# Kernel optimization log

Hardware: AMD Instinct MI355X
Metric: run time of the kernel (lower is better)

## Reference

```python
import jax, jax.numpy as jnp
import numpy as np

N_UNITS = 2048
N_INPUTS = 16
BATCH = 64
T = 512
PROP_EXC = 0.8
TAU = 5.0
GLOBAL_NOISE_LEVEL = 0.01
NOISE_CONST = float(np.sqrt(2.0 * GLOBAL_NOISE_LEVEL / TAU))


def setup_inputs() -> dict:
    key = jax.random.key(0)
    ks = jax.random.split(key, 7)
    inputs = jax.random.normal(ks[0], (BATCH, N_INPUTS, T), dtype=jnp.float32)
    noise = NOISE_CONST * jax.random.normal(ks[1], (T, BATCH, N_UNITS), dtype=jnp.float32)
    # parameters (match torch.rand-based init distributions)
    inp = jax.random.uniform(ks[2], (N_INPUTS, N_UNITS), dtype=jnp.float32)
    Wrecnon = (jax.random.uniform(ks[3], (N_UNITS, N_UNITS), dtype=jnp.float32) - 1.0) / N_UNITS
    Wrecdale = jax.random.uniform(ks[4], (N_UNITS, N_UNITS), dtype=jnp.float32) / N_UNITS
    out_w = jax.random.uniform(ks[5], (N_UNITS, 1), dtype=jnp.float32)
    alpha = jnp.array([0.5], dtype=jnp.float32)
    n_exc = int(PROP_EXC * N_UNITS)
    sdale = jnp.where(jnp.arange(N_UNITS) < n_exc, 1.0, -1.0).astype(jnp.float32)  # diag of Sdale
    return {"inputs": inputs, "noise": noise, "inp": inp, "Wrecnon": Wrecnon,
            "Wrecdale": Wrecdale, "out_w": out_w, "alpha": alpha, "sdale": sdale}


def reference(inputs, noise, inp, Wrecnon, Wrecdale, out_w, alpha, sdale):
    prop_old = 1.0 - 1.0 / TAU
    prop_new = 1.0 / TAU
    use_alpha = jnp.clip(alpha, 0.0, 1.0)  # Hardtanh(0, 1)
    # Wsum = a * |Wrecdale| @ diag(sdale) + (1 - a) * Wrecnon
    Wsum = use_alpha * (jnp.abs(Wrecdale) * sdale[None, :]) + (1.0 - use_alpha) * Wrecnon
    inp_abs = jnp.abs(inp)  # [n_inputs, n_units]
    x_seq = jnp.transpose(inputs, (2, 0, 1))  # [T, B, n_inputs]

    def step(activity, xs):
        x_t, n_t = xs
        # matmul(Wsum, relu(act)[..., None]).squeeze() == relu(act) @ Wsum.T
        drive = jnp.maximum(activity, 0.0) @ Wsum.T + x_t @ inp_abs
        activity = prop_old * activity + prop_new * drive + n_t
        return activity, None

    activity0 = jnp.zeros((inputs.shape[0], Wsum.shape[0]), dtype=inputs.dtype)
    activity, _ = jax.lax.scan(step, activity0, (x_seq, noise))
    output = (activity @ out_w)[:, 0]  # [B]
    return output, activity
```

## Files before the change

kernel.cpp:

```cpp
#include <hip/hip_runtime.h>

#define N_UNITS 2048
#define N_IN 16
#define BATCH 64
#define T_STEPS 512

typedef __attribute__((ext_vector_type(8))) short bf16x8;
typedef __attribute__((ext_vector_type(4))) float f32x4;
typedef __attribute__((ext_vector_type(4))) unsigned short u16x4;

#define AP_OFF   0
#define BX_OFF   17039360
#define BR0_OFF  21233664
#define BR1_OFF  21757952
#define ACT_OFF  22282240

__device__ __forceinline__ unsigned short f2bf(float f) {
  unsigned int u = __float_as_uint(f);
  u += 0x7FFFu + ((u >> 16) & 1u);
  return (unsigned short)(u >> 16);
}
__device__ __forceinline__ float bf2f(unsigned short h) {
  return __uint_as_float(((unsigned int)h) << 16);
}

__global__ __launch_bounds__(256) void k_packA(const float* __restrict__ Wd,
                                               const float* __restrict__ Wn,
                                               const float* __restrict__ sdale,
                                               const float* __restrict__ alphap,
                                               const float* __restrict__ inp,
                                               unsigned short* __restrict__ Ap) {
  int wid = blockIdx.x * 4 + (threadIdx.x >> 6);
  int l = threadIdx.x & 63;
  int mtile = wid / 130;
  int c = wid - mtile * 130;
  float a = fminf(fmaxf(alphap[0], 0.f), 1.f);
  float bb = 1.f - a;
  int u = mtile * 16 + (l & 15);
  int kb = (l >> 4) * 8;
  unsigned short o[8];
  if (c < 128) {
    int k0 = (c & 63) * 32 + kb;
    bool lo = (c >= 64);
    const float* wd = Wd + (size_t)u * 2048 + k0;
    const float* wn = Wn + (size_t)u * 2048 + k0;
    const float* sd = sdale + k0;
#pragma unroll
    for (int j = 0; j < 8; ++j) {
      float v = a * fabsf(wd[j]) * sd[j] + bb * wn[j];
      unsigned short h = f2bf(v);
      o[j] = lo ? f2bf(v - bf2f(h)) : h;
    }
  } else {
    int cw = c - 128;
#pragma unroll
    for (int j = 0; j < 8; ++j) {
      int kk = cw * 32 + kb + j;
      int sect = kk >> 4, i = kk & 15;
      float v = fabsf(inp[i * 2048 + u]);
      unsigned short h = f2bf(v);
      o[j] = (sect == 3) ? (unsigned short)0
                         : (sect == 2 ? f2bf(v - bf2f(h)) : h);
    }
  }
  unsigned short* dst = Ap + ((size_t)wid * 64 + l) * 8;
  *(u16x4*)dst = u16x4{o[0], o[1], o[2], o[3]};
  *(u16x4*)(dst + 4) = u16x4{o[4], o[5], o[6], o[7]};
}

__global__ __launch_bounds__(256) void k_packBx(const float* __restrict__ inputs,
                                                unsigned short* __restrict__ Bx) {
  int wid = blockIdx.x * 4 + (threadIdx.x >> 6);
  int l = threadIdx.x & 63;
  int t = wid >> 3, r = wid & 7, nt = r >> 1, c2 = r & 1;
  int b = nt * 16 + (l & 15);
  int kb = (l >> 4) * 8;
  unsigned short o[8];
#pragma unroll
  for (int j = 0; j < 8; ++j) {
    int kk = c2 * 32 + kb + j;
    int sect = kk >> 4, i = kk & 15;
    float x = inputs[(size_t)b * 8192 + i * 512 + t];
    unsigned short h = f2bf(x);
    o[j] = (sect == 3) ? (unsigned short)0
                       : (sect == 1 ? f2bf(x - bf2f(h)) : h);
  }
  unsigned short* dst = Bx + ((size_t)wid * 64 + l) * 8;
  *(u16x4*)dst = u16x4{o[0], o[1], o[2], o[3]};
  *(u16x4*)(dst + 4) = u16x4{o[4], o[5], o[6], o[7]};
}

__global__ __launch_bounds__(256) void k_zero(float4* __restrict__ p) {
  p[blockIdx.x * 256 + threadIdx.x] = make_float4(0.f, 0.f, 0.f, 0.f);
}

#define MFMA(A, B, C) __builtin_amdgcn_mfma_f32_16x16x32_bf16(A, B, C, 0, 0, 0)

__global__ __launch_bounds__(256, 1) void k_step(
    const unsigned short* __restrict__ Ap,
    const unsigned short* __restrict__ Brc,
    unsigned short* __restrict__ Brn,
    const unsigned short* __restrict__ Bxt,
    const float* __restrict__ noise_t,
    float* __restrict__ act) {
  const int tid = threadIdx.x;
  const int w = __builtin_amdgcn_readfirstlane(tid >> 6);
  const int l = tid & 63;
  const int u0 = blockIdx.x * 16;

  const unsigned short* Aw = Ap + ((size_t)blockIdx.x * 130) * 512 + l * 8;
  const unsigned short* Bl = Brc + l * 8;

  f32x4 acc0 = {0.f, 0.f, 0.f, 0.f}, acc1 = acc0, acc2 = acc0, acc3 = acc0;

  const int cbase = w * 16;
#pragma unroll 2
  for (int cc = 0; cc < 16; ++cc) {
    const int c = cbase + cc;
    bf16x8 ah = *(const bf16x8*)(Aw + (size_t)c * 512);
    bf16x8 al = *(const bf16x8*)(Aw + (size_t)(64 + c) * 512);
    bf16x8 bh0 = *(const bf16x8*)(Bl + (size_t)(0 * 128 + c) * 512);
    bf16x8 bh1 = *(const bf16x8*)(Bl + (size_t)(1 * 128 + c) * 512);
    bf16x8 bh2 = *(const bf16x8*)(Bl + (size_t)(2 * 128 + c) * 512);
    bf16x8 bh3 = *(const bf16x8*)(Bl + (size_t)(3 * 128 + c) * 512);
    bf16x8 bl0 = *(const bf16x8*)(Bl + (size_t)(0 * 128 + 64 + c) * 512);
    bf16x8 bl1 = *(const bf16x8*)(Bl + (size_t)(1 * 128 + 64 + c) * 512);
    bf16x8 bl2 = *(const bf16x8*)(Bl + (size_t)(2 * 128 + 64 + c) * 512);
    bf16x8 bl3 = *(const bf16x8*)(Bl + (size_t)(3 * 128 + 64 + c) * 512);
    acc0 = MFMA(ah, bh0, acc0);
    acc1 = MFMA(ah, bh1, acc1);
    acc2 = MFMA(ah, bh2, acc2);
    acc3 = MFMA(ah, bh3, acc3);
    acc0 = MFMA(ah, bl0, acc0);
    acc1 = MFMA(ah, bl1, acc1);
    acc2 = MFMA(ah, bl2, acc2);
    acc3 = MFMA(ah, bl3, acc3);
    acc0 = MFMA(al, bh0, acc0);
    acc1 = MFMA(al, bh1, acc1);
    acc2 = MFMA(al, bh2, acc2);
    acc3 = MFMA(al, bh3, acc3);
  }
  if (w < 2) {
    bf16x8 ax = *(const bf16x8*)(Aw + (size_t)(128 + w) * 512);
    bf16x8 bx0 = *(const bf16x8*)(Bxt + (size_t)(0 * 2 + w) * 512 + l * 8);
    bf16x8 bx1 = *(const bf16x8*)(Bxt + (size_t)(1 * 2 + w) * 512 + l * 8);
    bf16x8 bx2 = *(const bf16x8*)(Bxt + (size_t)(2 * 2 + w) * 512 + l * 8);
    bf16x8 bx3 = *(const bf16x8*)(Bxt + (size_t)(3 * 2 + w) * 512 + l * 8);
    acc0 = MFMA(ax, bx0, acc0);
    acc1 = MFMA(ax, bx1, acc1);
    acc2 = MFMA(ax, bx2, acc2);
    acc3 = MFMA(ax, bx3, acc3);
  }

  const int b = tid >> 2;
  const int ub = (tid & 3) * 4;
  const int ug = u0 + ub;
  const float4 nz = *(const float4*)(noise_t + (size_t)b * 2048 + ug);
  const float4 ao = *(const float4*)(act + (size_t)b * 2048 + ug);

  __shared__ float red[4][16][66];
  const int rl = l & 15, rh = l >> 4;
#pragma unroll
  for (int q = 0; q < 4; ++q) {
    red[w][rh * 4 + q][0 + rl] = acc0[q];
    red[w][rh * 4 + q][16 + rl] = acc1[q];
    red[w][rh * 4 + q][32 + rl] = acc2[q];
    red[w][rh * 4 + q][48 + rl] = acc3[q];
  }
  __syncthreads();

  float dr[4];
#pragma unroll
  for (int i = 0; i < 4; ++i)
    dr[i] = red[0][ub + i][b] + red[1][ub + i][b] +
            red[2][ub + i][b] + red[3][ub + i][b];

  float4 an;
  an.x = 0.8f * ao.x + 0.2f * dr[0] + nz.x;
  an.y = 0.8f * ao.y + 0.2f * dr[1] + nz.y;
  an.z = 0.8f * ao.z + 0.2f * dr[2] + nz.z;
  an.w = 0.8f * ao.w + 0.2f * dr[3] + nz.w;
  *(float4*)(act + (size_t)b * 2048 + ug) = an;

  float rr[4] = {fmaxf(an.x, 0.f), fmaxf(an.y, 0.f),
                 fmaxf(an.z, 0.f), fmaxf(an.w, 0.f)};
  u16x4 hv, lv;
#pragma unroll
  for (int i = 0; i < 4; ++i) {
    unsigned short h = f2bf(rr[i]);
    hv[i] = h;
    lv[i] = f2bf(rr[i] - bf2f(h));
  }
  const int c = ug >> 5;
  const int kk = ug & 31;
  const int lane_b = (b & 15) + 16 * (kk >> 3);
  const int j = kk & 7;
  const int nt = b >> 4;
  unsigned short* dst = Brn + ((size_t)(nt * 128 + c) * 64 + lane_b) * 8 + j;
  *(u16x4*)dst = hv;
  *(u16x4*)(dst + 32768) = lv;
}

__global__ __launch_bounds__(256) void k_trans(const float4* __restrict__ act,
                                               float4* __restrict__ out) {
  int idx = blockIdx.x * 256 + threadIdx.x;
  out[idx] = act[idx];
}

__global__ __launch_bounds__(256) void k_out(const float* __restrict__ act,
                                             const float* __restrict__ outw,
                                             float* __restrict__ out) {
  __shared__ float red[256];
  int b = blockIdx.x, tid = threadIdx.x;
  float p = 0.f;
  for (int u = tid; u < N_UNITS; u += 256)
    p = fmaf(act[b * N_UNITS + u], outw[u], p);
  red[tid] = p;
  __syncthreads();
  for (int s = 128; s > 0; s >>= 1) {
    if (tid < s) red[tid] += red[tid + s];
    __syncthreads();
  }
  if (tid == 0) out[b] = red[0];
}

extern "C" void kernel_launch(void* const* d_in, const int* in_sizes, int n_in,
                              void* d_out, int out_size, void* d_ws, size_t ws_size,
                              hipStream_t stream) {
  const float* inputs = (const float*)d_in[0];
  const float* noise  = (const float*)d_in[1];
  const float* inp    = (const float*)d_in[2];
  const float* Wn     = (const float*)d_in[3];
  const float* Wd     = (const float*)d_in[4];
  const float* outw   = (const float*)d_in[5];
  const float* alpha  = (const float*)d_in[6];
  const float* sdale  = (const float*)d_in[7];
  float* out = (float*)d_out;

  char* ws = (char*)d_ws;
  unsigned short* Ap  = (unsigned short*)(ws + AP_OFF);
  unsigned short* Bx  = (unsigned short*)(ws + BX_OFF);
  unsigned short* Br0 = (unsigned short*)(ws + BR0_OFF);
  unsigned short* Br1 = (unsigned short*)(ws + BR1_OFF);
  float* act          = (float*)(ws + ACT_OFF);

  k_packA<<<4160, 256, 0, stream>>>(Wd, Wn, sdale, alpha, inp, Ap);
  k_packBx<<<1024, 256, 0, stream>>>(inputs, Bx);
  k_zero<<<384, 256, 0, stream>>>((float4*)(ws + BR0_OFF));

  unsigned short* rb[2] = {Br0, Br1};
  for (int t = 0; t < T_STEPS; ++t) {
    k_step<<<128, 256, 0, stream>>>(Ap, rb[t & 1], rb[(t & 1) ^ 1],
                                    Bx + (size_t)t * 4096,
                                    noise + (size_t)t * 131072, act);
  }

  k_trans<<<128, 256, 0, stream>>>((const float4*)act, (float4*)(out + BATCH));
  k_out<<<64, 256, 0, stream>>>(act, outw, out);
}
```

Before: 6.766 ms.

## Replace per-timestep kernel launches with persistent kernel and grid barrier

```diff
diff --git a/kernel.cpp b/kernel.cpp
--- a/kernel.cpp
+++ b/kernel.cpp
@@ -4,6 +4,7 @@
 #define N_IN 16
 #define BATCH 64
 #define T_STEPS 512
+#define NBLK 128
 
 typedef __attribute__((ext_vector_type(8))) short bf16x8;
 typedef __attribute__((ext_vector_type(4))) float f32x4;
@@ -90,115 +91,147 @@
   *(u16x4*)(dst + 4) = u16x4{o[4], o[5], o[6], o[7]};
 }
 
-__global__ __launch_bounds__(256) void k_zero(float4* __restrict__ p) {
+__global__ __launch_bounds__(256) void k_zero(float4* __restrict__ p,
+                                              unsigned* __restrict__ bar) {
   p[blockIdx.x * 256 + threadIdx.x] = make_float4(0.f, 0.f, 0.f, 0.f);
+  if (blockIdx.x == 0 && threadIdx.x == 0) { bar[0] = 0u; bar[1] = 0u; }
 }
 
 #define MFMA(A, B, C) __builtin_amdgcn_mfma_f32_16x16x32_bf16(A, B, C, 0, 0, 0)
 
-__global__ __launch_bounds__(256, 1) void k_step(
+__global__ __launch_bounds__(256, 1) void k_persist(
     const unsigned short* __restrict__ Ap,
-    const unsigned short* __restrict__ Brc,
-    unsigned short* __restrict__ Brn,
-    const unsigned short* __restrict__ Bxt,
-    const float* __restrict__ noise_t,
-    float* __restrict__ act) {
+    unsigned short* __restrict__ Br0,
+    unsigned short* __restrict__ Br1,
+    const unsigned short* __restrict__ Bx,
+    const float* __restrict__ noise,
+    float* __restrict__ act,
+    unsigned* __restrict__ bar) {
   const int tid = threadIdx.x;
   const int w = __builtin_amdgcn_readfirstlane(tid >> 6);
   const int l = tid & 63;
   const int u0 = blockIdx.x * 16;
 
   const unsigned short* Aw = Ap + ((size_t)blockIdx.x * 130) * 512 + l * 8;
-  const unsigned short* Bl = Brc + l * 8;
-
-  f32x4 acc0 = {0.f, 0.f, 0.f, 0.f}, acc1 = acc0, acc2 = acc0, acc3 = acc0;
-
-  const int cbase = w * 16;
+  __shared__ float red[4][16][66];
+
+  for (int t = 0; t < T_STEPS; ++t) {
+    const unsigned short* Brc = (t & 1) ? Br1 : Br0;
+    unsigned short* Brn = (t & 1) ? Br0 : Br1;
+    const unsigned short* Bxt = Bx + (size_t)t * 4096;
+    const float* noise_t = noise + (size_t)t * 131072;
+    const unsigned short* Bl = Brc + l * 8;
+
+    f32x4 acc0 = {0.f, 0.f, 0.f, 0.f}, acc1 = acc0, acc2 = acc0, acc3 = acc0;
+
+    const int cbase = w * 16;
 #pragma unroll 2
-  for (int cc = 0; cc < 16; ++cc) {
-    const int c = cbase + cc;
-    bf16x8 ah = *(const bf16x8*)(Aw + (size_t)c * 512);
-    bf16x8 al = *(const bf16x8*)(Aw + (size_t)(64 + c) * 512);
-    bf16x8 bh0 = *(const bf16x8*)(Bl + (size_t)(0 * 128 + c) * 512);
-    bf16x8 bh1 = *(const bf16x8*)(Bl + (size_t)(1 * 128 + c) * 512);
-    bf16x8 bh2 = *(const bf16x8*)(Bl + (size_t)(2 * 128 + c) * 512);
-    bf16x8 bh3 = *(const bf16x8*)(Bl + (size_t)(3 * 128 + c) * 512);
-    bf16x8 bl0 = *(const bf16x8*)(Bl + (size_t)(0 * 128 + 64 + c) * 512);
-    bf16x8 bl1 = *(const bf16x8*)(Bl + (size_t)(1 * 128 + 64 + c) * 512);
-    bf16x8 bl2 = *(const bf16x8*)(Bl + (size_t)(2 * 128 + 64 + c) * 512);
-    bf16x8 bl3 = *(const bf16x8*)(Bl + (size_t)(3 * 128 + 64 + c) * 512);
-    acc0 = MFMA(ah, bh0, acc0);
-    acc1 = MFMA(ah, bh1, acc1);
-    acc2 = MFMA(ah, bh2, acc2);
-    acc3 = MFMA(ah, bh3, acc3);
-    acc0 = MFMA(ah, bl0, acc0);
-    acc1 = MFMA(ah, bl1, acc1);
-    acc2 = MFMA(ah, bl2, acc2);
-    acc3 = MFMA(ah, bl3, acc3);
-    acc0 = MFMA(al, bh0, acc0);
-    acc1 = MFMA(al, bh1, acc1);
-    acc2 = MFMA(al, bh2, acc2);
-    acc3 = MFMA(al, bh3, acc3);
-  }
-  if (w < 2) {
-    bf16x8 ax = *(const bf16x8*)(Aw + (size_t)(128 + w) * 512);
-    bf16x8 bx0 = *(const bf16x8*)(Bxt + (size_t)(0 * 2 + w) * 512 + l * 8);
-    bf16x8 bx1 = *(const bf16x8*)(Bxt + (size_t)(1 * 2 + w) * 512 + l * 8);
-    bf16x8 bx2 = *(const bf16x8*)(Bxt + (size_t)(2 * 2 + w) * 512 + l * 8);
-    bf16x8 bx3 = *(const bf16x8*)(Bxt + (size_t)(3 * 2 + w) * 512 + l * 8);
-    acc0 = MFMA(ax, bx0, acc0);
-    acc1 = MFMA(ax, bx1, acc1);
-    acc2 = MFMA(ax, bx2, acc2);
-    acc3 = MFMA(ax, bx3, acc3);
-  }
-
-  const int b = tid >> 2;
-  const int ub = (tid & 3) * 4;
-  const int ug = u0 + ub;
-  const float4 nz = *(const float4*)(noise_t + (size_t)b * 2048 + ug);
-  const float4 ao = *(const float4*)(act + (size_t)b * 2048 + ug);
-
-  __shared__ float red[4][16][66];
-  const int rl = l & 15, rh = l >> 4;
-#pragma unroll
-  for (int q = 0; q < 4; ++q) {
-    red[w][rh * 4 + q][0 + rl] = acc0[q];
-    red[w][rh * 4 + q][16 + rl] = acc1[q];
-    red[w][rh * 4 + q][32 + rl] = acc2[q];
-    red[w][rh * 4 + q][48 + rl] = acc3[q];
-  }
-  __syncthreads();
-
-  float dr[4];
-#pragma unroll
-  for (int i = 0; i < 4; ++i)
-    dr[i] = red[0][ub + i][b] + red[1][ub + i][b] +
-            red[2][ub + i][b] + red[3][ub + i][b];
-
-  float4 an;
-  an.x = 0.8f * ao.x + 0.2f * dr[0] + nz.x;
-  an.y = 0.8f * ao.y + 0.2f * dr[1] + nz.y;
-  an.z = 0.8f * ao.z + 0.2f * dr[2] + nz.z;
-  an.w = 0.8f * ao.w + 0.2f * dr[3] + nz.w;
-  *(float4*)(act + (size_t)b * 2048 + ug) = an;
-
-  float rr[4] = {fmaxf(an.x, 0.f), fmaxf(an.y, 0.f),
-                 fmaxf(an.z, 0.f), fmaxf(an.w, 0.f)};
-  u16x4 hv, lv;
-#pragma unroll
-  for (int i = 0; i < 4; ++i) {
-    unsigned short h = f2bf(rr[i]);
-    hv[i] = h;
-    lv[i] = f2bf(rr[i] - bf2f(h));
-  }
-  const int c = ug >> 5;
-  const int kk = ug & 31;
-  const int lane_b = (b & 15) + 16 * (kk >> 3);
-  const int j = kk & 7;
-  const int nt = b >> 4;
-  unsigned short* dst = Brn + ((size_t)(nt * 128 + c) * 64 + lane_b) * 8 + j;
-  *(u16x4*)dst = hv;
-  *(u16x4*)(dst + 32768) = lv;
+    for (int cc = 0; cc < 16; ++cc) {
+      const int c = cbase + cc;
+      bf16x8 ah = *(const bf16x8*)(Aw + (size_t)c * 512);
+      bf16x8 al = *(const bf16x8*)(Aw + (size_t)(64 + c) * 512);
+      bf16x8 bh0 = *(const bf16x8*)(Bl + (size_t)(0 * 128 + c) * 512);
+      bf16x8 bh1 = *(const bf16x8*)(Bl + (size_t)(1 * 128 + c) * 512);
+      bf16x8 bh2 = *(const bf16x8*)(Bl + (size_t)(2 * 128 + c) * 512);
+      bf16x8 bh3 = *(const bf16x8*)(Bl + (size_t)(3 * 128 + c) * 512);
+      bf16x8 bl0 = *(const bf16x8*)(Bl + (size_t)(0 * 128 + 64 + c) * 512);
+      bf16x8 bl1 = *(const bf16x8*)(Bl + (size_t)(1 * 128 + 64 + c) * 512);
+      bf16x8 bl2 = *(const bf16x8*)(Bl + (size_t)(2 * 128 + 64 + c) * 512);
+      bf16x8 bl3 = *(const bf16x8*)(Bl + (size_t)(3 * 128 + 64 + c) * 512);
+      acc0 = MFMA(ah, bh0, acc0);
+      acc1 = MFMA(ah, bh1, acc1);
+      acc2 = MFMA(ah, bh2, acc2);
+      acc3 = MFMA(ah, bh3, acc3);
+      acc0 = MFMA(ah, bl0, acc0);
+      acc1 = MFMA(ah, bl1, acc1);
+      acc2 = MFMA(ah, bl2, acc2);
+      acc3 = MFMA(ah, bl3, acc3);
+      acc0 = MFMA(al, bh0, acc0);
+      acc1 = MFMA(al, bh1, acc1);
+      acc2 = MFMA(al, bh2, acc2);
+      acc3 = MFMA(al, bh3, acc3);
+    }
+    if (w < 2) {
+      bf16x8 ax = *(const bf16x8*)(Aw + (size_t)(128 + w) * 512);
+      bf16x8 bx0 = *(const bf16x8*)(Bxt + (size_t)(0 * 2 + w) * 512 + l * 8);
+      bf16x8 bx1 = *(const bf16x8*)(Bxt + (size_t)(1 * 2 + w) * 512 + l * 8);
+      bf16x8 bx2 = *(const bf16x8*)(Bxt + (size_t)(2 * 2 + w) * 512 + l * 8);
+      bf16x8 bx3 = *(const bf16x8*)(Bxt + (size_t)(3 * 2 + w) * 512 + l * 8);
+      acc0 = MFMA(ax, bx0, acc0);
+      acc1 = MFMA(ax, bx1, acc1);
+      acc2 = MFMA(ax, bx2, acc2);
+      acc3 = MFMA(ax, bx3, acc3);
+    }
+
+    const int b = tid >> 2;
+    const int ub = (tid & 3) * 4;
+    const int ug = u0 + ub;
+    const float4 nz = *(const float4*)(noise_t + (size_t)b * 2048 + ug);
+    const float4 ao = *(const float4*)(act + (size_t)b * 2048 + ug);
+
+    const int rl = l & 15, rh = l >> 4;
+    __syncthreads();
+#pragma unroll
+    for (int q = 0; q < 4; ++q) {
+      red[w][rh * 4 + q][0 + rl] = acc0[q];
+      red[w][rh * 4 + q][16 + rl] = acc1[q];
+      red[w][rh * 4 + q][32 + rl] = acc2[q];
+      red[w][rh * 4 + q][48 + rl] = acc3[q];
+    }
+    __syncthreads();
+
+    float dr[4];
+#pragma unroll
+    for (int i = 0; i < 4; ++i)
+      dr[i] = red[0][ub + i][b] + red[1][ub + i][b] +
+              red[2][ub + i][b] + red[3][ub + i][b];
+
+    float4 an;
+    an.x = 0.8f * ao.x + 0.2f * dr[0] + nz.x;
+    an.y = 0.8f * ao.y + 0.2f * dr[1] + nz.y;
+    an.z = 0.8f * ao.z + 0.2f * dr[2] + nz.z;
+    an.w = 0.8f * ao.w + 0.2f * dr[3] + nz.w;
+    *(float4*)(act + (size_t)b * 2048 + ug) = an;
+
+    float rr[4] = {fmaxf(an.x, 0.f), fmaxf(an.y, 0.f),
+                   fmaxf(an.z, 0.f), fmaxf(an.w, 0.f)};
+    u16x4 hv, lv;
+#pragma unroll
+    for (int i = 0; i < 4; ++i) {
+      unsigned short h = f2bf(rr[i]);
+      hv[i] = h;
+      lv[i] = f2bf(rr[i] - bf2f(h));
+    }
+    const int c = ug >> 5;
+    const int kk = ug & 31;
+    const int lane_b = (b & 15) + 16 * (kk >> 3);
+    const int j = kk & 7;
+    const int nt = b >> 4;
+    unsigned short* dst = Brn + ((size_t)(nt * 128 + c) * 64 + lane_b) * 8 + j;
+    *(u16x4*)dst = hv;
+    *(u16x4*)(dst + 32768) = lv;
+
+    __syncthreads();
+    if (tid == 0) {
+      __threadfence();
+      unsigned g = __hip_atomic_load(&bar[1], __ATOMIC_RELAXED,
+                                     __HIP_MEMORY_SCOPE_AGENT);
+      unsigned a = __hip_atomic_fetch_add(&bar[0], 1u, __ATOMIC_ACQ_REL,
+                                          __HIP_MEMORY_SCOPE_AGENT);
+      if (a == NBLK - 1) {
+        __hip_atomic_store(&bar[0], 0u, __ATOMIC_RELAXED,
+                           __HIP_MEMORY_SCOPE_AGENT);
+        __hip_atomic_store(&bar[1], g + 1u, __ATOMIC_RELEASE,
+                           __HIP_MEMORY_SCOPE_AGENT);
+      } else {
+        while (__hip_atomic_load(&bar[1], __ATOMIC_ACQUIRE,
+                                 __HIP_MEMORY_SCOPE_AGENT) == g)
+          __builtin_amdgcn_s_sleep(2);
+      }
+    }
+    __syncthreads();
+    __threadfence();
+  }
 }
 
 __global__ __launch_bounds__(256) void k_trans(const float4* __restrict__ act,
@@ -243,17 +276,13 @@
   unsigned short* Br0 = (unsigned short*)(ws + BR0_OFF);
   unsigned short* Br1 = (unsigned short*)(ws + BR1_OFF);
   float* act          = (float*)(ws + ACT_OFF);
+  unsigned* bar       = (unsigned*)d_out;
 
   k_packA<<<4160, 256, 0, stream>>>(Wd, Wn, sdale, alpha, inp, Ap);
   k_packBx<<<1024, 256, 0, stream>>>(inputs, Bx);
-  k_zero<<<384, 256, 0, stream>>>((float4*)(ws + BR0_OFF));
-
-  unsigned short* rb[2] = {Br0, Br1};
-  for (int t = 0; t < T_STEPS; ++t) {
-    k_step<<<128, 256, 0, stream>>>(Ap, rb[t & 1], rb[(t & 1) ^ 1],
-                                    Bx + (size_t)t * 4096,
-                                    noise + (size_t)t * 131072, act);
-  }
+  k_zero<<<384, 256, 0, stream>>>((float4*)(ws + BR0_OFF), bar);
+
+  k_persist<<<NBLK, 256, 0, stream>>>(Ap, Br0, Br1, Bx, noise, act, bar);
 
   k_trans<<<128, 256, 0, stream>>>((const float4*)act, (float4*)(out + BATCH));
   k_out<<<64, 256, 0, stream>>>(act, outw, out);
```

Result: slower. 20.96 ms (+209.7%).
